# Kernel tuning notes

Measured on AMD Instinct MI355X. Metric: run time of the kernel, lower is better.

Reference implementation:

```python
import jax, jax.numpy as jnp
import numpy as np

NUM_CLASSES = 200
NPC = 10  # prototypes per class
P = NUM_CLASSES * NPC
D = 128


def setup_inputs() -> dict:
    key = jax.random.key(0)
    kx, kp = jax.random.split(key)
    x = jax.random.normal(kx, (16, D, 56, 56), dtype=jnp.float32)
    prototypes = jax.random.normal(kp, (1, P, D), dtype=jnp.float32)
    return {"x": x, "prototypes": prototypes}


def _cdist(a, b):
    # a: [B, N, D], b: [1, P, D] -> [B, N, P] Euclidean distances
    a2 = jnp.sum(a * a, axis=-1, keepdims=True)            # [B, N, 1]
    b2 = jnp.sum(b * b, axis=-1)[:, None, :]               # [1, 1, P]
    ab = jnp.einsum('bnd,zpd->bnp', a, b)                  # [B, N, P]
    d2 = jnp.maximum(a2 + b2 - 2.0 * ab, 0.0)
    return jnp.sqrt(d2)


def reference(x, prototypes):
    B, C, H, W = x.shape
    xf = x.reshape(B, C, H * W).transpose(0, 2, 1)         # [B, N, D]
    distances = _cdist(xf, prototypes)                     # [B, N, P]
    similarity = jnp.log((distances + 1.0) / (distances + 1e-7))
    max_similarity = jnp.max(similarity, axis=1)           # [B, P]
    min_distances = jnp.min(distances, axis=1)             # [B, P]
    arg_min = jnp.argmin(distances, axis=1)                # [B, P]
    min_features = jnp.take_along_axis(xf, arg_min[:, :, None], axis=1)  # [B, P, D]
    min_distances_per_class = min_distances.reshape(B, NUM_CLASSES, NPC)
    return (max_similarity, min_distances_per_class, min_features)
```

## Files before the change

### kernel.cpp

```cpp
#include <hip/hip_runtime.h>
#include <hip/hip_bf16.h>
#include <cmath>

#define DDIM 128
#define NPTS 3136
#define NCHUNK 196
#define QCHUNK 49
#define BATCH 16
#define PROT 2000
#define PPAD 2048

typedef __attribute__((ext_vector_type(8))) short bf16x8;
typedef __attribute__((ext_vector_type(4))) float f32x4;
typedef __attribute__((ext_vector_type(4))) unsigned int u32x4;

#define WS_X2   0
#define WS_K1   50176
#define WS_K2   181248
#define WS_PT   312320
#define WS_XT   443392
#define WS_XFT  3654656
#define WS_MID  ((size_t)3654656 * 4)
#define WS_BIG  ((size_t)10077184 * 4)

__device__ inline unsigned short bf16rn(float a) {
    unsigned u = __float_as_uint(a);
    unsigned r = u + 0x7FFFu + ((u >> 16) & 1u);
    return (unsigned short)(r >> 16);
}

__device__ __forceinline__ void gload_lds16(const void* g, void* l) {
    __builtin_amdgcn_global_load_lds(
        (const __attribute__((address_space(1))) void*)g,
        (__attribute__((address_space(3))) void*)l, 16, 0, 0);
}
__device__ __forceinline__ void gload_lds4(const void* g, void* l) {
    __builtin_amdgcn_global_load_lds(
        (const __attribute__((address_space(1))) void*)g,
        (__attribute__((address_space(3))) void*)l, 4, 0, 0);
}

__global__ __launch_bounds__(256)
void pp_fused(const float* __restrict__ x, const float* __restrict__ proto,
              unsigned short* __restrict__ xt, unsigned short* __restrict__ pt,
              float* __restrict__ x2, float* __restrict__ xfT) {
    int tid = threadIdx.x;
    if (blockIdx.x == 49) {
        int by = blockIdx.y;
        if (by >= 8) return;
        int p = by * 256 + tid;
        int ps = min(p, PROT - 1);
        const float* src = proto + (size_t)ps * DDIM;
        unsigned short* dst = pt + (size_t)p * 128;
        for (int j = 0; j < DDIM; ++j) dst[j] = bf16rn(src[j]);
        return;
    }
    __shared__ float xs[DDIM][64];
    int b = blockIdx.y;
    int n0 = blockIdx.x * 64;
    {
        int r = tid >> 4, c = tid & 15;
        #pragma unroll
        for (int it = 0; it < 8; ++it) {
            int row = it * 16 + r;
            f32x4 v = *(const f32x4*)(x + ((size_t)(b * DDIM + row)) * NPTS + n0 + c * 4);
            *(f32x4*)(&xs[row][c * 4]) = v;
        }
    }
    __syncthreads();
    if (tid < 64) {
        float s = 0.f;
        #pragma unroll 8
        for (int d = 0; d < DDIM; ++d) { float v = xs[d][tid]; s = fmaf(v, v, s); }
        x2[b * NPTS + n0 + tid] = (s + 512.0f) * 512.0f;
    }
    int n = tid & 63, kk = tid >> 6;
    int nl = n & 15, ci = (n0 + n) >> 4;
    unsigned int hw[16];
    #pragma unroll
    for (int j = 0; j < 16; ++j) {
        unsigned short h0 = bf16rn(xs[kk * 32 + 2 * j][n]);
        unsigned short h1 = bf16rn(xs[kk * 32 + 2 * j + 1][n]);
        hw[j] = (unsigned)h0 | ((unsigned)h1 << 16);
    }
    char* cb = (char*)xt + ((size_t)b * NCHUNK + ci) * 4096;
    #pragma unroll
    for (int g = 0; g < 4; ++g)
        *(u32x4*)(cb + kk * 1024 + g * 256 + nl * 16) = *(u32x4*)(&hw[g * 4]);
    if (xfT) {
        float* fo = xfT + ((size_t)b * NPTS + n0 + n) * DDIM + kk * 32;
        #pragma unroll
        for (int g = 0; g < 8; ++g) {
            f32x4 v;
            v[0] = xs[kk * 32 + g * 4 + 0][n];
            v[1] = xs[kk * 32 + g * 4 + 1][n];
            v[2] = xs[kk * 32 + g * 4 + 2][n];
            v[3] = xs[kk * 32 + g * 4 + 3][n];
            *(f32x4*)(fo + g * 4) = v;
        }
    }
}

__global__ __launch_bounds__(256, 4)
void proto_mfma(const unsigned short* __restrict__ xt,
                const unsigned short* __restrict__ pt,
                const float* __restrict__ x2,
                unsigned* __restrict__ k1w, unsigned* __restrict__ k2w) {
    __shared__ __align__(16) char LDS[20480];
    float* x2s = (float*)LDS;
    char*  AsB = LDS + 4096;

    int lid = blockIdx.x;
    int sid = (lid & 7) * 128 + (lid >> 3);
    int b = sid >> 6;
    int rest = sid & 63;
    int pbase = (rest >> 2) * 128;
    int q = rest & 3;

    int tid = threadIdx.x;
    int lane = tid & 63, psg = tid >> 6;
    int l15 = lane & 15, lg = lane >> 4;

    const unsigned short* bpa = pt + (size_t)(pbase + psg * 32 + l15) * 128 + lg * 8;
    const unsigned short* bpb = bpa + (size_t)16 * 128;
    bf16x8 Ba0 = *(const bf16x8*)(bpa);
    bf16x8 Ba1 = *(const bf16x8*)(bpa + 32);
    bf16x8 Ba2 = *(const bf16x8*)(bpa + 64);
    bf16x8 Ba3 = *(const bf16x8*)(bpa + 96);
    bf16x8 Bb0 = *(const bf16x8*)(bpb);
    bf16x8 Bb1 = *(const bf16x8*)(bpb + 32);
    bf16x8 Bb2 = *(const bf16x8*)(bpb + 64);
    bf16x8 Bb3 = *(const bf16x8*)(bpb + 96);

    const char* srcBase = (const char*)xt + ((size_t)b * NCHUNK + q * QCHUNK) * 4096;
    const char* aread = AsB + lane * 16;
    const int qOfs = q * (QCHUNK * 16);
    const int nbBase = qOfs + lg * 4;

    unsigned K1a = 0xFFFFFFFFu, K2a = 0xFFFFFFFFu;
    unsigned K1b = 0xFFFFFFFFu, K2b = 0xFFFFFFFFu;

    {
        const float* xsrc = x2 + (size_t)b * NPTS + qOfs;
        #pragma unroll
        for (int r = 0; r < 4; ++r)
            gload_lds4(xsrc + min(r * 256 + psg * 64 + lane, QCHUNK * 16 - 1),
                       (char*)x2s + (r * 256 + psg * 64) * 4);
    }
    #pragma unroll
    for (int r = 0; r < 3; ++r)
        gload_lds16(srcBase + (size_t)r * 4096 + psg * 1024 + (size_t)lane * 16,
                    AsB + r * 4096 + psg * 1024);

#define PMF_TRACK(ACC, XV, NB, K1, K2)                                              \
        _Pragma("unroll")                                                           \
        for (int rr = 0; rr < 4; ++rr) {                                            \
            float f = fmaf((ACC)[rr], -1024.f, (XV)[rr]);                           \
            unsigned k = ((unsigned)f << 12) | (unsigned)((NB) + rr);               \
            K2 = min(K2, max(K1, k));                                               \
            K1 = min(K1, k);                                                        \
        }

#define PMF_BODY(T, U)                                                              \
    {                                                                               \
        asm volatile("s_waitcnt vmcnt(2)" ::: "memory");                            \
        __builtin_amdgcn_s_barrier();                                               \
        int cln = (T) + 3;                                                          \
        cln = cln > QCHUNK - 1 ? QCHUNK - 1 : cln;                                  \
        gload_lds16(srcBase + (size_t)cln * 4096 + psg * 1024 + (size_t)lane * 16,  \
                    AsB + (((U) + 3) & 3) * 4096 + psg * 1024);                     \
        f32x4 xv = *(const f32x4*)&x2s[(T) * 16 + lg * 4];                          \
        const char* ar = aread + (U) * 4096;                                        \
        bf16x8 A0 = *(const bf16x8*)(ar);                                           \
        bf16x8 A1 = *(const bf16x8*)(ar + 1024);                                    \
        bf16x8 A2 = *(const bf16x8*)(ar + 2048);                                    \
        bf16x8 A3 = *(const bf16x8*)(ar + 3072);                                    \
        f32x4 accA = {0.f, 0.f, 0.f, 0.f};                                          \
        f32x4 accB = {0.f, 0.f, 0.f, 0.f};                                          \
        __builtin_amdgcn_s_setprio(1);                                              \
        accA = __builtin_amdgcn_mfma_f32_16x16x32_bf16(A0, Ba0, accA, 0, 0, 0);     \
        accB = __builtin_amdgcn_mfma_f32_16x16x32_bf16(A0, Bb0, accB, 0, 0, 0);     \
        accA = __builtin_amdgcn_mfma_f32_16x16x32_bf16(A1, Ba1, accA, 0, 0, 0);     \
        accB = __builtin_amdgcn_mfma_f32_16x16x32_bf16(A1, Bb1, accB, 0, 0, 0);     \
        accA = __builtin_amdgcn_mfma_f32_16x16x32_bf16(A2, Ba2, accA, 0, 0, 0);     \
        accB = __builtin_amdgcn_mfma_f32_16x16x32_bf16(A2, Bb2, accB, 0, 0, 0);     \
        accA = __builtin_amdgcn_mfma_f32_16x16x32_bf16(A3, Ba3, accA, 0, 0, 0);     \
        accB = __builtin_amdgcn_mfma_f32_16x16x32_bf16(A3, Bb3, accB, 0, 0, 0);     \
        __builtin_amdgcn_s_setprio(0);                                              \
        int nb = nbBase + (T) * 16;                                                 \
        PMF_TRACK(accA, xv, nb, K1a, K2a)                                           \
        PMF_TRACK(accB, xv, nb, K1b, K2b)                                           \
    }

    #pragma unroll 1
    for (int t0 = 0; t0 < 48; t0 += 4) {
        PMF_BODY(t0 + 0, 0)
        PMF_BODY(t0 + 1, 1)
        PMF_BODY(t0 + 2, 2)
        PMF_BODY(t0 + 3, 3)
    }
    PMF_BODY(48, 0)
#undef PMF_BODY
#undef PMF_TRACK

    #pragma unroll
    for (int m = 16; m <= 32; m <<= 1) {
        unsigned c1a = (unsigned)__shfl_xor((int)K1a, m, 64);
        unsigned c2a = (unsigned)__shfl_xor((int)K2a, m, 64);
        unsigned wa  = max(K1a, c1a);
        K1a = min(K1a, c1a);
        K2a = min(wa, min(K2a, c2a));
        unsigned c1b = (unsigned)__shfl_xor((int)K1b, m, 64);
        unsigned c2b = (unsigned)__shfl_xor((int)K2b, m, 64);
        unsigned wb  = max(K1b, c1b);
        K1b = min(K1b, c1b);
        K2b = min(wb, min(K2b, c2b));
    }
    if (lg == 0) {
        size_t o = ((size_t)b * 4 + q) * PPAD + pbase + psg * 32 + l15;
        k1w[o] = K1a;
        k2w[o] = K2a;
        k1w[o + 16] = K1b;
        k2w[o + 16] = K2b;
    }
}

template<int MODE>
__global__ __launch_bounds__(256)
void fixup(const float* __restrict__ x, const float* __restrict__ xfT,
           const float* __restrict__ proto,
           const unsigned* __restrict__ k1w, const unsigned* __restrict__ k2w,
           float* __restrict__ out) {
    int tid = threadIdx.x;
    int lane = tid & 63, wv = tid >> 6;
    long long pair = (long long)blockIdx.x * 4 + wv;
    if (pair >= (long long)BATCH * PROT) return;
    int b = (int)(pair / PROT), p = (int)(pair % PROT);
    unsigned a0 = k1w[((size_t)b * 4 + 0) * PPAD + p];
    unsigned a1 = k1w[((size_t)b * 4 + 1) * PPAD + p];
    unsigned a2 = k1w[((size_t)b * 4 + 2) * PPAD + p];
    unsigned a3 = k1w[((size_t)b * 4 + 3) * PPAD + p];
    unsigned c0 = k2w[((size_t)b * 4 + 0) * PPAD + p];
    unsigned c1 = k2w[((size_t)b * 4 + 1) * PPAD + p];
    unsigned c2 = k2w[((size_t)b * 4 + 2) * PPAD + p];
    unsigned c3 = k2w[((size_t)b * 4 + 3) * PPAD + p];
    int cand[4];
    cand[0] = (int)(min(a0, a1) & 0xFFFu);
    cand[1] = (int)(min(max(a0, a1), min(c0, c1)) & 0xFFFu);
    cand[2] = (int)(min(a2, a3) & 0xFFFu);
    cand[3] = (int)(min(max(a2, a3), min(c2, c3)) & 0xFFFu);

    int d0 = lane, d1 = lane + 64;
    float pa0 = proto[(size_t)p * DDIM + d0], pa1 = proto[(size_t)p * DDIM + d1];
    float sp2 = pa0 * pa0 + pa1 * pa1;
    float f0[4], f1[4], sxp[4], sx2[4];
    #pragma unroll
    for (int c = 0; c < 4; ++c) {
        int n = cand[c];
        float v0, v1;
        if (MODE == 0) {
            const float* f = xfT + ((size_t)b * NPTS + n) * DDIM;
            v0 = f[d0]; v1 = f[d1];
        } else {
            const float* xb = x + (size_t)b * DDIM * NPTS;
            v0 = xb[(size_t)d0 * NPTS + n]; v1 = xb[(size_t)d1 * NPTS + n];
        }
        f0[c] = v0; f1[c] = v1;
        sxp[c] = v0 * pa0 + v1 * pa1;
        sx2[c] = v0 * v0 + v1 * v1;
    }
    #pragma unroll
    for (int m = 1; m < 64; m <<= 1) {
        sp2 += __shfl_xor(sp2, m, 64);
        #pragma unroll
        for (int c = 0; c < 4; ++c) {
            sxp[c] += __shfl_xor(sxp[c], m, 64);
            sx2[c] += __shfl_xor(sx2[c], m, 64);
        }
    }
    float bd = 3e38f; int bn = 0x7FFFFFFF; int bc = 0;
    #pragma unroll
    for (int c = 0; c < 4; ++c) {
        float d2 = fmaxf(sx2[c] + sp2 - 2.f * sxp[c], 0.f);
        bool w = (d2 < bd) || (d2 == bd && cand[c] < bn);
        bd = w ? d2 : bd;
        bn = w ? cand[c] : bn;
        bc = w ? c : bc;
    }
    float dm = sqrtf(bd);
    float sim = logf((dm + 1.0f) / (dm + 1e-7f));
    if (lane == 0) {
        out[(size_t)b * PROT + p] = sim;
        out[(size_t)BATCH * PROT + (size_t)b * PROT + p] = dm;
    }
    float o0 = f0[0], o1 = f1[0];
    #pragma unroll
    for (int c = 1; c < 4; ++c) {
        o0 = (bc == c) ? f0[c] : o0;
        o1 = (bc == c) ? f1[c] : o1;
    }
    float* fo = out + (size_t)2 * BATCH * PROT + ((size_t)b * PROT + p) * DDIM;
    fo[d0] = o0;
    fo[d1] = o1;
}

#define TP 64
#define TN 64
__global__ void p2_kernel(const float* __restrict__ proto, float* __restrict__ p2) {
    int p = blockIdx.x * blockDim.x + threadIdx.x;
    if (p >= PROT) return;
    const float4* pr = reinterpret_cast<const float4*>(proto + (size_t)p * DDIM);
    float s = 0.f;
    #pragma unroll
    for (int i = 0; i < DDIM / 4; ++i) {
        float4 v = pr[i];
        s += v.x * v.x + v.y * v.y + v.z * v.z + v.w * v.w;
    }
    p2[p] = s;
}
__global__ void x2_kernel(const float* __restrict__ x, float* __restrict__ x2) {
    int idx = blockIdx.x * blockDim.x + threadIdx.x;
    if (idx >= BATCH * NPTS) return;
    int b = idx / NPTS, n = idx - b * NPTS;
    const float* xp = x + (size_t)b * DDIM * NPTS + n;
    float s = 0.f;
    #pragma unroll 8
    for (int d = 0; d < DDIM; ++d) { float v = xp[(size_t)d * NPTS]; s += v * v; }
    x2[idx] = s;
}
__global__ __launch_bounds__(256, 2)
void proto_main(const float* __restrict__ x, const float* __restrict__ proto,
                const float* __restrict__ p2, const float* __restrict__ x2,
                float* __restrict__ out) {
    __shared__ __align__(16) float xs[DDIM][TN];
    __shared__ __align__(16) float pst[DDIM][TP];
    __shared__ float p2s[TP];
    __shared__ float x2s[TN];
    __shared__ float red_d2[16][TP];
    __shared__ int   red_n[16][TP];
    __shared__ int   bestn_s[TP];
    const int b = blockIdx.y;
    const int pbase = blockIdx.x * TP;
    const int tid = threadIdx.x;
    {
        #pragma unroll
        for (int it = 0; it < (TP * DDIM / 4) / 256; ++it) {
            int idx = it * 256 + tid;
            int p = idx / (DDIM / 4);
            int dq = idx - p * (DDIM / 4);
            int gp = min(pbase + p, PROT - 1);
            float4 v = reinterpret_cast<const float4*>(proto)[(size_t)gp * (DDIM / 4) + dq];
            pst[dq * 4 + 0][p] = v.x; pst[dq * 4 + 1][p] = v.y;
            pst[dq * 4 + 2][p] = v.z; pst[dq * 4 + 3][p] = v.w;
        }
        if (tid < TP) p2s[tid] = p2[min(pbase + tid, PROT - 1)];
    }
    const int tn = tid >> 4;
    const int tp = tid & 15;
    float best[4]; int bestn[4];
    #pragma unroll
    for (int j = 0; j < 4; ++j) { best[j] = 1e30f; bestn[j] = 0; }
    for (int n0 = 0; n0 < NPTS; n0 += TN) {
        __syncthreads();
        {
            int r = tid >> 4, c = tid & 15;
            #pragma unroll
            for (int it = 0; it < 8; ++it) {
                int row = it * 16 + r;
                float4 v = *reinterpret_cast<const float4*>(
                    x + ((size_t)(b * DDIM + row)) * NPTS + n0 + c * 4);
                *reinterpret_cast<float4*>(&xs[row][c * 4]) = v;
            }
        }
        if (tid < TN) x2s[tid] = x2[b * NPTS + n0 + tid];
        __syncthreads();
        float acc[4][4];
        #pragma unroll
        for (int i = 0; i < 4; ++i)
            #pragma unroll
            for (int j = 0; j < 4; ++j) acc[i][j] = 0.f;
        #pragma unroll 16
        for (int d = 0; d < DDIM; ++d) {
            const float4 a = *reinterpret_cast<const float4*>(&xs[d][tn * 4]);
            const float4 bv = *reinterpret_cast<const float4*>(&pst[d][tp * 4]);
            const float av[4] = {a.x, a.y, a.z, a.w};
            const float bw[4] = {bv.x, bv.y, bv.z, bv.w};
            #pragma unroll
            for (int i = 0; i < 4; ++i)
                #pragma unroll
                for (int j = 0; j < 4; ++j) acc[i][j] = fmaf(av[i], bw[j], acc[i][j]);
        }
        #pragma unroll
        for (int i = 0; i < 4; ++i) {
            float xv = x2s[tn * 4 + i];
            int n = n0 + tn * 4 + i;
            #pragma unroll
            for (int j = 0; j < 4; ++j) {
                float d2 = xv + p2s[tp * 4 + j] - 2.0f * acc[i][j];
                if (d2 < best[j]) { best[j] = d2; bestn[j] = n; }
            }
        }
    }
    #pragma unroll
    for (int j = 0; j < 4; ++j) {
        red_d2[tn][tp * 4 + j] = best[j];
        red_n[tn][tp * 4 + j] = bestn[j];
    }
    __syncthreads();
    if (tid < TP) {
        float bd = red_d2[0][tid]; int bn = red_n[0][tid];
        #pragma unroll
        for (int t = 1; t < 16; ++t) {
            float dv = red_d2[t][tid]; int nv = red_n[t][tid];
            if (dv < bd || (dv == bd && nv < bn)) { bd = dv; bn = nv; }
        }
        int gp = pbase + tid;
        if (gp < PROT) {
            float d2c = fmaxf(bd, 0.f);
            float dmin = sqrtf(d2c);
            float sim = logf((dmin + 1.0f) / (dmin + 1e-7f));
            out[(size_t)b * PROT + gp] = sim;
            out[(size_t)BATCH * PROT + (size_t)b * PROT + gp] = dmin;
        }
        bestn_s[tid] = bn;
    }
    __syncthreads();
    {
        int pl = tid >> 2, dbase = (tid & 3) * 32;
        int gp = pbase + pl;
        if (gp < PROT) {
            int n = bestn_s[pl];
            float* dst = out + (size_t)2 * BATCH * PROT + ((size_t)(b * PROT + gp)) * DDIM + dbase;
            const float* src = x + ((size_t)(b * DDIM + dbase)) * NPTS + n;
            #pragma unroll 8
            for (int d = 0; d < 32; ++d) dst[d] = src[(size_t)d * NPTS];
        }
    }
}

extern "C" void kernel_launch(void* const* d_in, const int* in_sizes, int n_in,
                              void* d_out, int out_size, void* d_ws, size_t ws_size,
                              hipStream_t stream) {
    const float* x = (const float*)d_in[0];
    const float* proto = (const float*)d_in[1];
    float* out = (float*)d_out;
    float* ws = (float*)d_ws;

    if (ws_size >= WS_MID) {
        bool big = (ws_size >= WS_BIG);
        float* x2 = ws + WS_X2;
        unsigned* k1w = (unsigned*)(ws + WS_K1);
        unsigned* k2w = (unsigned*)(ws + WS_K2);
        unsigned short* pt = (unsigned short*)(ws + WS_PT);
        unsigned short* xt = (unsigned short*)(ws + WS_XT);
        float* xfT = big ? (ws + WS_XFT) : nullptr;

        pp_fused<<<dim3(50, BATCH), 256, 0, stream>>>(x, proto, xt, pt, x2, xfT);
        proto_mfma<<<1024, 256, 0, stream>>>(xt, pt, x2, k1w, k2w);
        if (big)
            fixup<0><<<(BATCH * PROT) / 4, 256, 0, stream>>>(x, xfT, proto, k1w, k2w, out);
        else
            fixup<1><<<(BATCH * PROT) / 4, 256, 0, stream>>>(x, nullptr, proto, k1w, k2w, out);
    } else {
        float* p2 = ws;
        float* x2 = ws + 2048;
        p2_kernel<<<(PROT + 255) / 256, 256, 0, stream>>>(proto, p2);
        x2_kernel<<<(BATCH * NPTS + 255) / 256, 256, 0, stream>>>(x, x2);
        dim3 grid((PROT + TP - 1) / TP, BATCH);
        proto_main<<<grid, 256, 0, stream>>>(x, proto, p2, x2, out);
    }
}
```

Before: 78.44 us.

## Split point range into eight chunks per block, doubling grid for occupancy

The MFMA distance kernel now splits each batch's 196 point chunks into 8 segments (25/24 chunks) instead of 4 segments of 49, doubling the grid to 2048 blocks and raising the launch-bounds occupancy hint to 8. The fixup kernel merges top-2 candidates across 8 partial results in a two-level tree, still yielding 4 candidates. Workspace offsets grow for the larger K1/K2 buffers. The aim is better latency hiding and load balance across CUs, at the cost of more partial-result traffic and more per-block prologue overhead (B-fragment loads repeated). Reducing to 4 candidates from 8 segments may drop true-minimum candidates that bf16 errors would have caught.

```diff
diff --git a/kernel.cpp b/kernel.cpp
--- a/kernel.cpp
+++ b/kernel.cpp
@@ -5,7 +5,6 @@
 #define DDIM 128
 #define NPTS 3136
 #define NCHUNK 196
-#define QCHUNK 49
 #define BATCH 16
 #define PROT 2000
 #define PPAD 2048
@@ -16,12 +15,12 @@
 
 #define WS_X2   0
 #define WS_K1   50176
-#define WS_K2   181248
-#define WS_PT   312320
-#define WS_XT   443392
-#define WS_XFT  3654656
-#define WS_MID  ((size_t)3654656 * 4)
-#define WS_BIG  ((size_t)10077184 * 4)
+#define WS_K2   312320
+#define WS_PT   574464
+#define WS_XT   705536
+#define WS_XFT  3916800
+#define WS_MID  ((size_t)3916800 * 4)
+#define WS_BIG  ((size_t)10339328 * 4)
 
 __device__ inline unsigned short bf16rn(float a) {
     unsigned u = __float_as_uint(a);
@@ -101,7 +100,7 @@
     }
 }
 
-__global__ __launch_bounds__(256, 4)
+__global__ __launch_bounds__(256, 8)
 void proto_mfma(const unsigned short* __restrict__ xt,
                 const unsigned short* __restrict__ pt,
                 const float* __restrict__ x2,
@@ -111,11 +110,14 @@
     char*  AsB = LDS + 4096;
 
     int lid = blockIdx.x;
-    int sid = (lid & 7) * 128 + (lid >> 3);
-    int b = sid >> 6;
-    int rest = sid & 63;
-    int pbase = (rest >> 2) * 128;
-    int q = rest & 3;
+    int sid = (lid & 7) * 256 + (lid >> 3);
+    int b = sid >> 7;
+    int rest = sid & 127;
+    int pbase = (rest >> 3) * 128;
+    int q8 = rest & 7;
+
+    int L = (q8 < 4) ? 25 : 24;
+    int start = (q8 < 4) ? q8 * 25 : 100 + (q8 - 4) * 24;
 
     int tid = threadIdx.x;
     int lane = tid & 63, psg = tid >> 6;
@@ -132,9 +134,9 @@
     bf16x8 Bb2 = *(const bf16x8*)(bpb + 64);
     bf16x8 Bb3 = *(const bf16x8*)(bpb + 96);
 
-    const char* srcBase = (const char*)xt + ((size_t)b * NCHUNK + q * QCHUNK) * 4096;
+    const char* srcBase = (const char*)xt + ((size_t)b * NCHUNK + start) * 4096;
     const char* aread = AsB + lane * 16;
-    const int qOfs = q * (QCHUNK * 16);
+    const int qOfs = start * 16;
     const int nbBase = qOfs + lg * 4;
 
     unsigned K1a = 0xFFFFFFFFu, K2a = 0xFFFFFFFFu;
@@ -143,8 +145,8 @@
     {
         const float* xsrc = x2 + (size_t)b * NPTS + qOfs;
         #pragma unroll
-        for (int r = 0; r < 4; ++r)
-            gload_lds4(xsrc + min(r * 256 + psg * 64 + lane, QCHUNK * 16 - 1),
+        for (int r = 0; r < 2; ++r)
+            gload_lds4(xsrc + min(r * 256 + psg * 64 + lane, L * 16 - 1),
                        (char*)x2s + (r * 256 + psg * 64) * 4);
     }
     #pragma unroll
@@ -166,7 +168,7 @@
         asm volatile("s_waitcnt vmcnt(2)" ::: "memory");                            \
         __builtin_amdgcn_s_barrier();                                               \
         int cln = (T) + 3;                                                          \
-        cln = cln > QCHUNK - 1 ? QCHUNK - 1 : cln;                                  \
+        cln = cln > L - 1 ? L - 1 : cln;                                            \
         gload_lds16(srcBase + (size_t)cln * 4096 + psg * 1024 + (size_t)lane * 16,  \
                     AsB + (((U) + 3) & 3) * 4096 + psg * 1024);                     \
         f32x4 xv = *(const f32x4*)&x2s[(T) * 16 + lg * 4];                          \
@@ -193,13 +195,15 @@
     }
 
     #pragma unroll 1
-    for (int t0 = 0; t0 < 48; t0 += 4) {
+    for (int t0 = 0; t0 < 24; t0 += 4) {
         PMF_BODY(t0 + 0, 0)
         PMF_BODY(t0 + 1, 1)
         PMF_BODY(t0 + 2, 2)
         PMF_BODY(t0 + 3, 3)
     }
-    PMF_BODY(48, 0)
+    if (L == 25) {
+        PMF_BODY(24, 0)
+    }
 #undef PMF_BODY
 #undef PMF_TRACK
 
@@ -217,7 +221,7 @@
         K2b = min(wb, min(K2b, c2b));
     }
     if (lg == 0) {
-        size_t o = ((size_t)b * 4 + q) * PPAD + pbase + psg * 32 + l15;
+        size_t o = ((size_t)b * 8 + q8) * PPAD + pbase + psg * 32 + l15;
         k1w[o] = K1a;
         k2w[o] = K2a;
         k1w[o + 16] = K1b;
@@ -236,27 +240,33 @@
     long long pair = (long long)blockIdx.x * 4 + wv;
     if (pair >= (long long)BATCH * PROT) return;
     int b = (int)(pair / PROT), p = (int)(pair % PROT);
-    unsigned a0 = k1w[((size_t)b * 4 + 0) * PPAD + p];
-    unsigned a1 = k1w[((size_t)b * 4 + 1) * PPAD + p];
-    unsigned a2 = k1w[((size_t)b * 4 + 2) * PPAD + p];
-    unsigned a3 = k1w[((size_t)b * 4 + 3) * PPAD + p];
-    unsigned c0 = k2w[((size_t)b * 4 + 0) * PPAD + p];
-    unsigned c1 = k2w[((size_t)b * 4 + 1) * PPAD + p];
-    unsigned c2 = k2w[((size_t)b * 4 + 2) * PPAD + p];
-    unsigned c3 = k2w[((size_t)b * 4 + 3) * PPAD + p];
+    unsigned a[8], c[8];
+    #pragma unroll
+    for (int qq = 0; qq < 8; ++qq) {
+        a[qq] = k1w[((size_t)b * 8 + qq) * PPAD + p];
+        c[qq] = k2w[((size_t)b * 8 + qq) * PPAD + p];
+    }
     int cand[4];
-    cand[0] = (int)(min(a0, a1) & 0xFFFu);
-    cand[1] = (int)(min(max(a0, a1), min(c0, c1)) & 0xFFFu);
-    cand[2] = (int)(min(a2, a3) & 0xFFFu);
-    cand[3] = (int)(min(max(a2, a3), min(c2, c3)) & 0xFFFu);
+    #pragma unroll
+    for (int h = 0; h < 2; ++h) {
+        int o = h * 4;
+        unsigned p1a = min(a[o], a[o + 1]);
+        unsigned p2a = min(max(a[o], a[o + 1]), min(c[o], c[o + 1]));
+        unsigned p1b = min(a[o + 2], a[o + 3]);
+        unsigned p2b = min(max(a[o + 2], a[o + 3]), min(c[o + 2], c[o + 3]));
+        unsigned h1 = min(p1a, p1b);
+        unsigned h2 = min(max(p1a, p1b), min(p2a, p2b));
+        cand[h * 2]     = (int)(h1 & 0xFFFu);
+        cand[h * 2 + 1] = (int)(h2 & 0xFFFu);
+    }
 
     int d0 = lane, d1 = lane + 64;
     float pa0 = proto[(size_t)p * DDIM + d0], pa1 = proto[(size_t)p * DDIM + d1];
     float sp2 = pa0 * pa0 + pa1 * pa1;
     float f0[4], f1[4], sxp[4], sx2[4];
     #pragma unroll
-    for (int c = 0; c < 4; ++c) {
-        int n = cand[c];
+    for (int cc = 0; cc < 4; ++cc) {
+        int n = cand[cc];
         float v0, v1;
         if (MODE == 0) {
             const float* f = xfT + ((size_t)b * NPTS + n) * DDIM;
@@ -265,27 +275,27 @@
             const float* xb = x + (size_t)b * DDIM * NPTS;
             v0 = xb[(size_t)d0 * NPTS + n]; v1 = xb[(size_t)d1 * NPTS + n];
         }
-        f0[c] = v0; f1[c] = v1;
-        sxp[c] = v0 * pa0 + v1 * pa1;
-        sx2[c] = v0 * v0 + v1 * v1;
+        f0[cc] = v0; f1[cc] = v1;
+        sxp[cc] = v0 * pa0 + v1 * pa1;
+        sx2[cc] = v0 * v0 + v1 * v1;
     }
     #pragma unroll
     for (int m = 1; m < 64; m <<= 1) {
         sp2 += __shfl_xor(sp2, m, 64);
         #pragma unroll
-        for (int c = 0; c < 4; ++c) {
-            sxp[c] += __shfl_xor(sxp[c], m, 64);
-            sx2[c] += __shfl_xor(sx2[c], m, 64);
+        for (int cc = 0; cc < 4; ++cc) {
+            sxp[cc] += __shfl_xor(sxp[cc], m, 64);
+            sx2[cc] += __shfl_xor(sx2[cc], m, 64);
         }
     }
     float bd = 3e38f; int bn = 0x7FFFFFFF; int bc = 0;
     #pragma unroll
-    for (int c = 0; c < 4; ++c) {
-        float d2 = fmaxf(sx2[c] + sp2 - 2.f * sxp[c], 0.f);
-        bool w = (d2 < bd) || (d2 == bd && cand[c] < bn);
+    for (int cc = 0; cc < 4; ++cc) {
+        float d2 = fmaxf(sx2[cc] + sp2 - 2.f * sxp[cc], 0.f);
+        bool w = (d2 < bd) || (d2 == bd && cand[cc] < bn);
         bd = w ? d2 : bd;
-        bn = w ? cand[c] : bn;
-        bc = w ? c : bc;
+        bn = w ? cand[cc] : bn;
+        bc = w ? cc : bc;
     }
     float dm = sqrtf(bd);
     float sim = logf((dm + 1.0f) / (dm + 1e-7f));
@@ -295,9 +305,9 @@
     }
     float o0 = f0[0], o1 = f1[0];
     #pragma unroll
-    for (int c = 1; c < 4; ++c) {
-        o0 = (bc == c) ? f0[c] : o0;
-        o1 = (bc == c) ? f1[c] : o1;
+    for (int cc = 1; cc < 4; ++cc) {
+        o0 = (bc == cc) ? f0[cc] : o0;
+        o1 = (bc == cc) ? f1[cc] : o1;
     }
     float* fo = out + (size_t)2 * BATCH * PROT + ((size_t)b * PROT + p) * DDIM;
     fo[d0] = o0;
@@ -456,7 +466,7 @@
         float* xfT = big ? (ws + WS_XFT) : nullptr;
 
         pp_fused<<<dim3(50, BATCH), 256, 0, stream>>>(x, proto, xt, pt, x2, xfT);
-        proto_mfma<<<1024, 256, 0, stream>>>(xt, pt, x2, k1w, k2w);
+        proto_mfma<<<2048, 256, 0, stream>>>(xt, pt, x2, k1w, k2w);
         if (big)
             fixup<0><<<(BATCH * PROT) / 4, 256, 0, stream>>>(x, xfT, proto, k1w, k2w, out);
         else
```

Measured after the change: 141.6 us. 1.8x slower.
